# Kernel optimization log

Hardware: AMD Instinct MI355X
Metric: run time of the kernel (lower is better)

Reference implementation:

```python
import jax, jax.numpy as jnp
import numpy as np

N, F, P, NT = 4096, 256, 5, 5  # agents, feat dim, n_persona, n_time_steps
EPS = 1e-8


def setup_inputs() -> dict:
    key = jax.random.key(0)
    ks = jax.random.split(key, 7)
    attributes = jax.random.normal(ks[0], (N, F), dtype=jnp.float32)
    edges = (jax.random.uniform(ks[1], (N, N)) < 0.01).astype(jnp.float32)
    persona = jax.random.uniform(ks[2], (NT, N, P), dtype=jnp.float32)
    T = jax.random.uniform(ks[3], (P,), dtype=jnp.float32) * 0.5 + 0.5  # keep temperature away from 0
    e = jax.random.uniform(ks[4], (P,), dtype=jnp.float32) + 0.5
    r = jax.random.uniform(ks[5], (P,), dtype=jnp.float32)
    W = jax.random.uniform(ks[6], (P,), dtype=jnp.float32) + 0.5
    return {"attributes": attributes, "edges": edges, "persona": persona,
            "T": T, "e": e, "r": r, "W": W, "times": 2}


def reference(attributes, edges, persona, T, e, r, W, times):
    p = persona[times]                      # [N, P] persona weights at this time step
    msg = edges @ attributes                # [N, F] message passing, shared across personas

    def body(acc, xs):
        idx, Ti, ei, ri, Wi, pi = xs        # pi: [N]
        feat = ri * attributes + (msg * Wi) * (1.0 - ri)          # [N, F]
        nf = feat / jnp.sqrt(jnp.sum(feat * feat, axis=1, keepdims=True))  # row L2 norm
        x = jnp.exp((nf @ nf.T) / (Ti + EPS)) * ei                 # [N, N]
        x = x / (jnp.max(x) + EPS)                                 # min-max scale (min=0)
        # (1 - exp(-2v)) / (1 + exp(-2v)) == tanh(v)
        tc = jnp.tanh(x) * pi[None, :]                              # column persona gating
        # i == 0 initializes edges_prob with tc, every i adds row-gated tc
        acc = acc + tc * pi[:, None] + jnp.where(idx == 0, 1.0, 0.0) * tc
        return acc, None

    acc0 = jnp.zeros((N, N), dtype=jnp.float32)
    out, _ = jax.lax.scan(body, acc0, (jnp.arange(P), T, e, r, W, p.T))
    return out
```

## Files before the change

kernel.cpp:

```cpp
#include <hip/hip_runtime.h>
#include <hip/hip_bf16.h>

#define N 4096
#define F 256
#define P 5
#define EPSV 1e-8f
#define BK 32
#define NSTEP (F / BK)
#define NTRI 2080
#define GRIDSZ 512
#define DDEG 12
#define NC (DDEG + 1)
#define PAN 16384
#define Q0OFF 49152
#define QSZ 10240
#define CFOFF 69632

typedef __attribute__((ext_vector_type(8))) short bf16x8;
typedef __attribute__((ext_vector_type(4))) float f32x4;
typedef __attribute__((ext_vector_type(2))) float f32x2;

__device__ __forceinline__ f32x4 mfma16(bf16x8 a, bf16x8 b, f32x4 c) {
    return __builtin_amdgcn_mfma_f32_16x16x32_bf16(a, b, c, 0, 0, 0);
}

__device__ __forceinline__ void gload16(const void* src, const char* ldsdst) {
    __builtin_amdgcn_global_load_lds(
        (const __attribute__((address_space(1))) void*)src,
        (__attribute__((address_space(3))) void*)ldsdst, 16, 0, 0);
}

__device__ __forceinline__ f32x2 sp(float x) { return (f32x2){x, x}; }

#define SB() __builtin_amdgcn_sched_barrier(0)
#define RAWBAR() do { SB(); __builtin_amdgcn_s_barrier(); SB(); } while (0)

__global__ __launch_bounds__(256, 4) void prep_kernel(
    const float* __restrict__ E, const float* __restrict__ A,
    const float* __restrict__ persona,
    const float* __restrict__ Tt, const float* __restrict__ ee,
    const float* __restrict__ rr, const float* __restrict__ Ww,
    const int* __restrict__ times,
    __hip_bfloat16* __restrict__ Abf, __hip_bfloat16* __restrict__ Mbf,
    float* __restrict__ qsoa, float* __restrict__ cstg, int* __restrict__ ctr) {
    __shared__ int cnt;
    __shared__ int list[1024];
    const int a = blockIdx.x;
    const int t = threadIdx.x;
    if (t == 0) cnt = 0;
    __syncthreads();
    const float4* erow = (const float4*)(E + (size_t)a * N);
    for (int b = t; b < N / 4; b += 256) {
        const float4 v = erow[b];
        if (v.x != 0.f) list[atomicAdd(&cnt, 1)] = 4 * b;
        if (v.y != 0.f) list[atomicAdd(&cnt, 1)] = 4 * b + 1;
        if (v.z != 0.f) list[atomicAdd(&cnt, 1)] = 4 * b + 2;
        if (v.w != 0.f) list[atomicAdd(&cnt, 1)] = 4 * b + 3;
    }
    __syncthreads();
    const int c = cnt;
    float s0 = 0.f, s1 = 0.f, s2 = 0.f, s3 = 0.f;
    float s4 = 0.f, s5 = 0.f, s6 = 0.f, s7 = 0.f;
    int j = 0;
    for (; j + 8 <= c; j += 8) {
        s0 += A[(size_t)list[j] * F + t];
        s1 += A[(size_t)list[j + 1] * F + t];
        s2 += A[(size_t)list[j + 2] * F + t];
        s3 += A[(size_t)list[j + 3] * F + t];
        s4 += A[(size_t)list[j + 4] * F + t];
        s5 += A[(size_t)list[j + 5] * F + t];
        s6 += A[(size_t)list[j + 6] * F + t];
        s7 += A[(size_t)list[j + 7] * F + t];
    }
    for (; j < c; ++j) s0 += A[(size_t)list[j] * F + t];
    const float mv = ((s0 + s1) + (s2 + s3)) + ((s4 + s5) + (s6 + s7));
    const float av = A[(size_t)a * F + t];
    Abf[(size_t)a * F + t] = __float2bfloat16(av);
    Mbf[(size_t)a * F + t] = __float2bfloat16(mv);

    float paa = av * av, pam = av * mv, pmm = mv * mv;
    #pragma unroll
    for (int o = 32; o > 0; o >>= 1) {
        paa += __shfl_down(paa, o);
        pam += __shfl_down(pam, o);
        pmm += __shfl_down(pmm, o);
    }
    __shared__ float s[3][4];
    const int wid = t >> 6;
    if ((t & 63) == 0) { s[0][wid] = paa; s[1][wid] = pam; s[2][wid] = pmm; }
    __syncthreads();
    if (t < P) {
        const float naa = s[0][0] + s[0][1] + s[0][2] + s[0][3];
        const float nam = s[1][0] + s[1][1] + s[1][2] + s[1][3];
        const float nmm = s[2][0] + s[2][1] + s[2][2] + s[2][3];
        const float Ti = Tt[t], ei = ee[t], ri = rr[t], Wi = Ww[t];
        const float wb = (1.f - ri) * Wi;
        const float n2 = ri * ri * naa + 2.f * ri * wb * nam + wb * wb * nmm;
        const float rn = rsqrtf(n2);
        const float p = persona[(size_t)(*times) * (size_t)N * P + (size_t)a * P + t];
        qsoa[(t * 4 + 0) * N + a] = ri * rn;
        qsoa[(t * 4 + 1) * N + a] = wb * rn;
        qsoa[(t * 4 + 2) * N + a] = p;
        qsoa[(t * 4 + 3) * N + a] = p + (t == 0 ? 1.f : 0.f);
        if (a == 0) {
            const float kk = 1.f / (Ti + EPSV);
            const float scf = ei / (ei * __expf(kk) + EPSV);
            float ch[NC];
            #pragma unroll
            for (int j2 = 0; j2 < NC; ++j2) ch[j2] = 0.f;
            for (int m = 0; m < 32; ++m) {
                const float th = 3.14159265358979323846f * (m + 0.5f) / 32.f;
                const float c1 = __cosf(th);
                const float x = scf * __expf(kk * 1.05f * c1);
                const float e2 = __expf(2.f * x);
                const float fm = 1.f - 2.f / (e2 + 1.f);
                float cjm1 = 1.f, cj = c1;
                ch[0] += fm;
                ch[1] += fm * c1;
                #pragma unroll
                for (int j2 = 2; j2 < NC; ++j2) {
                    const float cn = 2.f * c1 * cj - cjm1;
                    ch[j2] += fm * cn;
                    cjm1 = cj;
                    cj = cn;
                }
            }
            #pragma unroll
            for (int j2 = 0; j2 < NC; ++j2) ch[j2] *= (j2 == 0 ? 1.f : 2.f) / 32.f;
            float mono[NC], Tp[NC], Tc[NC], Tn[NC];
            const float is = 1.f / 1.05f;
            #pragma unroll
            for (int k2 = 0; k2 < NC; ++k2) {
                mono[k2] = 0.f; Tp[k2] = 0.f; Tc[k2] = 0.f; Tn[k2] = 0.f;
            }
            Tp[0] = 1.f;
            Tc[1] = is;
            #pragma unroll
            for (int k2 = 0; k2 < NC; ++k2) mono[k2] += ch[0] * Tp[k2] + ch[1] * Tc[k2];
            for (int j2 = 2; j2 < NC; ++j2) {
                #pragma unroll
                for (int k2 = 0; k2 < NC; ++k2)
                    Tn[k2] = 2.f * is * (k2 ? Tc[k2 - 1] : 0.f) - Tp[k2];
                #pragma unroll
                for (int k2 = 0; k2 < NC; ++k2) mono[k2] += ch[j2] * Tn[k2];
                #pragma unroll
                for (int k2 = 0; k2 < NC; ++k2) { Tp[k2] = Tc[k2]; Tc[k2] = Tn[k2]; }
            }
            #pragma unroll
            for (int k2 = 0; k2 < NC; ++k2) cstg[t * NC + k2] = mono[k2];
        }
    }
    if (a == 0 && t == 0) *ctr = GRIDSZ;
}

__global__ __launch_bounds__(512) void gram_kernel(
    const __hip_bfloat16* __restrict__ Abf, const __hip_bfloat16* __restrict__ Mbf,
    const float* __restrict__ qsoa, const float* __restrict__ cstg,
    int* __restrict__ ctr, float* __restrict__ out) {
    __shared__ __align__(16) char smem[69904];
    __shared__ int snext;

    const int t = threadIdx.x;
    const int lane = t & 63;
    const int w = t >> 6;
    const int wr = w >> 1;
    const int wc = w & 1;

    const int sslot = (lane & 3) ^ ((lane >> 3) & 3);
    const int srowoff = (w & 1) * 32 + (lane >> 2);
    const int ldsp = (w >> 1) * 4096 + (w & 1) * 2048;
    const __hip_bfloat16* smat = ((w >> 1) & 1) ? Mbf : Abf;

    const int frow = lane & 15;
    const int fg = lane >> 4;
    const int jr = fg << 2;
    const int rdslot = (fg ^ ((frow >> 1) & 3)) << 4;
    const int aoff = (wr * 16 + frow) * 64 + rdslot;
    const int coff0 = (wc * 32 + frow) * 64 + rdslot;
    const int coff1 = (wc * 32 + 16 + frow) * 64 + rdslot;
    const float* cfs = (const float*)(smem + CFOFF);

    #define DECODE(id, oby, obx) do {                                     \
        const int bid_ = ((id) & 7) * 260 + ((id) >> 3);                  \
        int bx_ = (int)((sqrtf(8.f * (float)bid_ + 1.f) - 1.f) * 0.5f);   \
        while ((bx_ + 1) * (bx_ + 2) / 2 <= bid_) ++bx_;                  \
        while (bx_ * (bx_ + 1) / 2 > bid_) --bx_;                         \
        (obx) = bx_;                                                      \
        (oby) = bid_ - bx_ * (bx_ + 1) / 2;                               \
    } while (0)

    #define PROLOGUE(r0_, c0_, qp_) do {                                  \
        const int sb_ = (w < 4) ? (r0_) : (c0_);                          \
        const __hip_bfloat16* ps_ =                                       \
            smat + (size_t)(sb_ + srowoff) * F + sslot * 8;               \
        gload16(ps_, smem + ldsp);                                        \
        gload16(ps_ + 16 * F, smem + ldsp + 1024);                        \
        gload16(ps_ + 32, smem + PAN + ldsp);                             \
        gload16(ps_ + 32 + 16 * F, smem + PAN + ldsp + 1024);             \
        const int qb_ = Q0OFF + (qp_) * QSZ;                              \
        if (w == 0) {                                                     \
            _Pragma("unroll")                                             \
            for (int it = 0; it < 5; ++it)                                \
                gload16(qsoa + (it * 4 + (lane >> 4)) * N + (r0_) +       \
                        (lane & 15) * 4, smem + qb_ + it * 1024);         \
        } else if (w == 1) {                                              \
            _Pragma("unroll")                                             \
            for (int it = 0; it < 5; ++it)                                \
                gload16(qsoa + (it * 4 + (lane >> 4)) * N + (c0_) +       \
                        (lane & 15) * 4, smem + qb_ + 5120 + it * 1024);  \
        }                                                                 \
        if (t == 0) snext = atomicAdd(ctr, 1);                            \
    } while (0)

    int raw = blockIdx.x;
    int by, bx;
    DECODE(raw, by, bx);
    int row0 = by << 6, col0 = bx << 6;
    int qpar = 0;
    int pend = 0;

    PROLOGUE(row0, col0, 0);
    if (w == 2 && lane < 17) gload16(cstg + lane * 4, smem + CFOFF);

    for (;;) {
        if (pend == 16) asm volatile("s_waitcnt vmcnt(16)" ::: "memory");
        else if (pend == 8) asm volatile("s_waitcnt vmcnt(8)" ::: "memory");
        else asm volatile("s_waitcnt vmcnt(0)" ::: "memory");
        RAWBAR();

        const int nxt = snext;

        const int sbc = (w < 4) ? row0 : col0;
        const __hip_bfloat16* psrc =
            smat + (size_t)(sbc + srowoff) * F + sslot * 8;

        f32x4 acc[4][2];
        #pragma unroll
        for (int g = 0; g < 4; ++g)
            #pragma unroll
            for (int n = 0; n < 2; ++n) acc[g][n] = (f32x4){0.f, 0.f, 0.f, 0.f};

        #pragma unroll
        for (int s = 0; s < NSTEP; ++s) {
            if (s + 2 < NSTEP) {
                const char* lb = smem + ((s + 2) % 3) * PAN + ldsp;
                gload16(psrc + (s + 2) * BK, lb);
                gload16(psrc + (s + 2) * BK + 16 * F, lb + 1024);
            }
            const char* base = smem + (s % 3) * PAN;
            const bf16x8 aA = *(const bf16x8*)(base + aoff);
            const bf16x8 aM = *(const bf16x8*)(base + 4096 + aoff);
            const bf16x8 bA0 = *(const bf16x8*)(base + 8192 + coff0);
            const bf16x8 bA1 = *(const bf16x8*)(base + 8192 + coff1);
            const bf16x8 bM0 = *(const bf16x8*)(base + 12288 + coff0);
            const bf16x8 bM1 = *(const bf16x8*)(base + 12288 + coff1);
            acc[0][0] = mfma16(aA, bA0, acc[0][0]);
            acc[0][1] = mfma16(aA, bA1, acc[0][1]);
            acc[1][0] = mfma16(aA, bM0, acc[1][0]);
            acc[1][1] = mfma16(aA, bM1, acc[1][1]);
            acc[2][0] = mfma16(aM, bA0, acc[2][0]);
            acc[2][1] = mfma16(aM, bA1, acc[2][1]);
            acc[3][0] = mfma16(aM, bM0, acc[3][0]);
            acc[3][1] = mfma16(aM, bM1, acc[3][1]);
            if (s + 1 < NSTEP) {
                if (s + 2 < NSTEP) asm volatile("s_waitcnt vmcnt(2)" ::: "memory");
                else asm volatile("s_waitcnt vmcnt(0)" ::: "memory");
                RAWBAR();
            }
        }

        RAWBAR();

        const bool have = (nxt < NTRI);
        int nby = 0, nbx = 0, nrow0 = 0, ncol0 = 0;
        if (have) {
            DECODE(nxt, nby, nbx);
            nrow0 = nby << 6;
            ncol0 = nbx << 6;
            PROLOGUE(nrow0, ncol0, qpar ^ 1);
        }

        const float* qlr = (const float*)(smem + Q0OFF + qpar * QSZ);
        const float* qlc = qlr + 1280;
        f32x2 o1[2][2], o2[2][2];
        #pragma unroll
        for (int n = 0; n < 2; ++n)
            #pragma unroll
            for (int jp = 0; jp < 2; ++jp) { o1[n][jp] = sp(0.f); o2[n][jp] = sp(0.f); }

        #pragma unroll
        for (int i = 0; i < P; ++i) {
            const int ib = i * 256;
            float cf[NC];
            #pragma unroll
            for (int k = 0; k < NC; ++k) cf[k] = cfs[i * NC + k];
            float cA[2], cB[2], cP0[2], cP1[2];
            #pragma unroll
            for (int n = 0; n < 2; ++n) {
                const int cr = wc * 32 + n * 16 + frow;
                cA[n]  = qlc[ib + cr];
                cB[n]  = qlc[ib + 64 + cr];
                cP0[n] = qlc[ib + 128 + cr];
                cP1[n] = qlc[ib + 192 + cr];
            }
            #pragma unroll
            for (int jp = 0; jp < 2; ++jp) {
                const int rrw = wr * 16 + jr + jp * 2;
                const f32x2 rA  = *(const f32x2*)&qlr[ib + rrw];
                const f32x2 rB  = *(const f32x2*)&qlr[ib + 64 + rrw];
                const f32x2 rP0 = *(const f32x2*)&qlr[ib + 128 + rrw];
                const f32x2 rP1 = *(const f32x2*)&qlr[ib + 192 + rrw];
                #pragma unroll
                for (int n = 0; n < 2; ++n) {
                    const f32x2 aAA = (f32x2){acc[0][n][2 * jp], acc[0][n][2 * jp + 1]};
                    const f32x2 aAM = (f32x2){acc[1][n][2 * jp], acc[1][n][2 * jp + 1]};
                    const f32x2 aMA = (f32x2){acc[2][n][2 * jp], acc[2][n][2 * jp + 1]};
                    const f32x2 aMM = (f32x2){acc[3][n][2 * jp], acc[3][n][2 * jp + 1]};
                    const f32x2 h0 = rA * aAA + rB * aMA;
                    const f32x2 h1 = rA * aAM + rB * aMM;
                    const f32x2 g2 = h0 * sp(cA[n]) + h1 * sp(cB[n]);
                    f32x2 f2 = sp(cf[DDEG]);
                    #pragma unroll
                    for (int k = DDEG - 1; k >= 0; --k) f2 = f2 * g2 + sp(cf[k]);
                    o1[n][jp] += (f2 * rP1) * sp(cP0[n]);
                    o2[n][jp] += (f2 * rP0) * sp(cP1[n]);
                }
            }
        }

        #pragma unroll
        for (int jp = 0; jp < 2; ++jp)
            #pragma unroll
            for (int cc = 0; cc < 2; ++cc) {
                const int gr = row0 + wr * 16 + jr + jp * 2 + cc;
                #pragma unroll
                for (int n = 0; n < 2; ++n) {
                    const int gc = col0 + wc * 32 + n * 16 + frow;
                    out[(size_t)gr * N + gc] = o1[n][jp][cc];
                }
            }
        if (by != bx) {
            #pragma unroll
            for (int jp = 0; jp < 2; ++jp)
                #pragma unroll
                for (int cc = 0; cc < 2; ++cc) {
                    const int gr = row0 + wr * 16 + jr + jp * 2 + cc;
                    #pragma unroll
                    for (int n = 0; n < 2; ++n) {
                        const int gc = col0 + wc * 32 + n * 16 + frow;
                        out[(size_t)gc * N + gr] = o2[n][jp][cc];
                    }
                }
            pend = 16;
        } else {
            pend = 8;
        }

        if (!have) break;
        raw = nxt; by = nby; bx = nbx; row0 = nrow0; col0 = ncol0; qpar ^= 1;
    }
    #undef PROLOGUE
    #undef DECODE
}

extern "C" void kernel_launch(void* const* d_in, const int* in_sizes, int n_in,
                              void* d_out, int out_size, void* d_ws, size_t ws_size,
                              hipStream_t stream) {
    const float* A = (const float*)d_in[0];
    const float* E = (const float*)d_in[1];
    const float* persona = (const float*)d_in[2];
    const float* T = (const float*)d_in[3];
    const float* e = (const float*)d_in[4];
    const float* r = (const float*)d_in[5];
    const float* W = (const float*)d_in[6];
    const int* times = (const int*)d_in[7];
    float* out = (float*)d_out;

    char* ws = (char*)d_ws;
    __hip_bfloat16* Abf = (__hip_bfloat16*)ws;
    __hip_bfloat16* Mbf = (__hip_bfloat16*)(ws + (2 << 20));
    float* qsoa = (float*)(ws + (4 << 20));
    float* cstg = (float*)(ws + (4 << 20) + 5 * 4 * N * 4);
    int* ctr = (int*)(ws + (4 << 20) + 5 * 4 * N * 4 + 512);

    prep_kernel<<<N, 256, 0, stream>>>(E, A, persona, T, e, r, W, times,
                                       Abf, Mbf, qsoa, cstg, ctr);
    gram_kernel<<<GRIDSZ, 512, 0, stream>>>(Abf, Mbf, qsoa, cstg, ctr, out);
}
```

Before: 82.27 us.

## Replace global tile counter with per-XCD chunked work queues and stealing

The single global atomic tile counter becomes eight counters, each owning a contiguous chunk of 260 triangular tiles. Blocks first draw from the counter selected by blockIdx&7, which on this part maps to one XCD, and steal from the other chunks once their own runs out. The intent is to keep neighbouring tiles on the same XCD for L2 reuse of the A/M panels and to cut contention on one atomic. In exchange, a block may issue up to eight serial atomics when it steals, and load balance near the end could be less even.

```diff
diff --git a/kernel.cpp b/kernel.cpp
--- a/kernel.cpp
+++ b/kernel.cpp
@@ -9,6 +9,7 @@
 #define NSTEP (F / BK)
 #define NTRI 2080
 #define GRIDSZ 512
+#define CHUNK 260
 #define DDEG 12
 #define NC (DDEG + 1)
 #define PAN 16384
@@ -150,7 +151,7 @@
             for (int k2 = 0; k2 < NC; ++k2) cstg[t * NC + k2] = mono[k2];
         }
     }
-    if (a == 0 && t == 0) *ctr = GRIDSZ;
+    if (a == 0 && t < 8) ctr[t] = t * CHUNK + GRIDSZ / 8;
 }
 
 __global__ __launch_bounds__(512) void gram_kernel(
@@ -165,6 +166,7 @@
     const int w = t >> 6;
     const int wr = w >> 1;
     const int wc = w & 1;
+    const int myx = (int)blockIdx.x & 7;
 
     const int sslot = (lane & 3) ^ ((lane >> 3) & 3);
     const int srowoff = (w & 1) * 32 + (lane >> 2);
@@ -180,13 +182,24 @@
     const int coff1 = (wc * 32 + 16 + frow) * 64 + rdslot;
     const float* cfs = (const float*)(smem + CFOFF);
 
+    #define STEAL() do {                                                  \
+        if (t == 0) {                                                     \
+            int got_ = -1;                                                \
+            for (int a2 = 0; a2 < 8; ++a2) {                              \
+                const int k2 = (myx + a2) & 7;                            \
+                const int v2 = atomicAdd(ctr + k2, 1);                    \
+                if (v2 < (k2 + 1) * CHUNK) { got_ = v2; break; }          \
+            }                                                             \
+            snext = got_;                                                 \
+        }                                                                 \
+    } while (0)
+
     #define DECODE(id, oby, obx) do {                                     \
-        const int bid_ = ((id) & 7) * 260 + ((id) >> 3);                  \
-        int bx_ = (int)((sqrtf(8.f * (float)bid_ + 1.f) - 1.f) * 0.5f);   \
-        while ((bx_ + 1) * (bx_ + 2) / 2 <= bid_) ++bx_;                  \
-        while (bx_ * (bx_ + 1) / 2 > bid_) --bx_;                         \
+        int bx_ = (int)((sqrtf(8.f * (float)(id) + 1.f) - 1.f) * 0.5f);   \
+        while ((bx_ + 1) * (bx_ + 2) / 2 <= (id)) ++bx_;                  \
+        while (bx_ * (bx_ + 1) / 2 > (id)) --bx_;                         \
         (obx) = bx_;                                                      \
-        (oby) = bid_ - bx_ * (bx_ + 1) / 2;                               \
+        (oby) = (id) - bx_ * (bx_ + 1) / 2;                               \
     } while (0)
 
     #define PROLOGUE(r0_, c0_, qp_) do {                                  \
@@ -209,15 +222,15 @@
                 gload16(qsoa + (it * 4 + (lane >> 4)) * N + (c0_) +       \
                         (lane & 15) * 4, smem + qb_ + 5120 + it * 1024);  \
         }                                                                 \
-        if (t == 0) snext = atomicAdd(ctr, 1);                            \
+        STEAL();                                                          \
     } while (0)
 
-    int raw = blockIdx.x;
+    const int first = myx * CHUNK + ((int)blockIdx.x >> 3);
     int by, bx;
-    DECODE(raw, by, bx);
+    DECODE(first, by, bx);
     int row0 = by << 6, col0 = bx << 6;
+    int pend = 0;
     int qpar = 0;
-    int pend = 0;
 
     PROLOGUE(row0, col0, 0);
     if (w == 2 && lane < 17) gload16(cstg + lane * 4, smem + CFOFF);
@@ -271,7 +284,7 @@
 
         RAWBAR();
 
-        const bool have = (nxt < NTRI);
+        const bool have = (nxt >= 0);
         int nby = 0, nbx = 0, nrow0 = 0, ncol0 = 0;
         if (have) {
             DECODE(nxt, nby, nbx);
@@ -357,10 +370,11 @@
         }
 
         if (!have) break;
-        raw = nxt; by = nby; bx = nbx; row0 = nrow0; col0 = ncol0; qpar ^= 1;
+        by = nby; bx = nbx; row0 = nrow0; col0 = ncol0; qpar ^= 1;
     }
     #undef PROLOGUE
     #undef DECODE
+    #undef STEAL
 }
 
 extern "C" void kernel_launch(void* const* d_in, const int* in_sizes, int n_in,
```

New measurement: 119.2 us. +44.8%, slower.
